# Kernel optimization log

Measured on AMD Instinct MI355X. Metric: run time of the kernel, lower is better.

Reference implementation:

```python
import jax, jax.numpy as jnp
import numpy as np

B, CIN, T = 16, 1024, 2000
BN, OUT, K = 512, 512, 3
DIL = (1, 2, 3)
NBR = len(DIL)
RED = 1
BN_EPS = 1e-5
STD_EPS = 0.01


def setup_inputs() -> dict:
    key = jax.random.key(0)
    ks = jax.random.split(key, 16)
    inp = {
        "x": jax.random.normal(ks[0], (B, CIN, T), dtype=jnp.float32),
        # BatchNorm1d(in_channels) params + running stats (inference mode)
        "bn1_gamma": jax.random.uniform(ks[1], (CIN,), minval=0.5, maxval=1.5),
        "bn1_beta": jax.random.normal(ks[2], (CIN,)) * 0.1,
        "bn1_mean": jax.random.normal(ks[3], (CIN,)) * 0.1,
        "bn1_var": jax.random.uniform(ks[4], (CIN,), minval=0.5, maxval=1.5),
        # linear1: in_channels -> bn_channels, no bias
        "W1": jax.random.normal(ks[5], (BN, CIN)) * (1.0 / np.sqrt(CIN)),
        # BatchNorm1d(bn_channels)
        "bn2_gamma": jax.random.uniform(ks[6], (BN,), minval=0.5, maxval=1.5),
        "bn2_beta": jax.random.normal(ks[7], (BN,)) * 0.1,
        "bn2_mean": jax.random.normal(ks[8], (BN,)) * 0.1,
        "bn2_var": jax.random.uniform(ks[9], (BN,), minval=0.5, maxval=1.5),
        # per-dilation TimeDelay weights [n_branch, OUT, BN, K] (bias=False)
        "conv_w": jax.random.normal(ks[10], (NBR, OUT, BN, K)) * (1.0 / np.sqrt(OUT)),
        # StatsSelect: linear1 (4C -> C//red), linear2 list (C//red -> C)
        "sel_W1": jax.random.normal(ks[11], (OUT // RED, 4 * OUT)) * (1.0 / np.sqrt(4 * OUT)),
        "sel_b1": jax.random.normal(ks[12], (OUT // RED,)) * 0.01,
        "sel_W2": jax.random.normal(ks[13], (NBR, OUT, OUT // RED)) * (1.0 / np.sqrt(OUT // RED)),
        "sel_b2": jax.random.normal(ks[14], (NBR, OUT)) * 0.01,
    }
    return inp


def _bn_relu(x, gamma, beta, mean, var):
    # inference BatchNorm1d over channel dim, then ReLU; x: [B, C, T]
    inv = gamma / jnp.sqrt(var + BN_EPS)
    y = x * inv[None, :, None] + (beta - mean * inv)[None, :, None]
    return jax.nn.relu(y)


def _forward(x, bn1_gamma, bn1_beta, bn1_mean, bn1_var, W1,
             bn2_gamma, bn2_beta, bn2_mean, bn2_var,
             conv_w, sel_W1, sel_b1, sel_W2, sel_b2):
    # bn_function: nonlinear1 -> linear1 (pointwise over channels)
    h = _bn_relu(x, bn1_gamma, bn1_beta, bn1_mean, bn1_var)  # [B, CIN, T]
    h = jnp.einsum('bct,oc->bot', h, W1)                      # [B, BN, T]
    h = _bn_relu(h, bn2_gamma, bn2_beta, bn2_mean, bn2_var)
    # multi-dilation TDNN branches (dilated conv1d with 'same' padding)
    pad = (K - 1) // 2
    outs = []
    for i, d in enumerate(DIL):
        y = jax.lax.conv_general_dilated(
            h, conv_w[i], window_strides=(1,), padding=[(pad * d, pad * d)],
            rhs_dilation=(d,), dimension_numbers=('NCH', 'OIH', 'NCH'))
        outs.append(y)
    f = jnp.stack(outs, axis=1)  # [B, n, OUT, T]
    xs = jnp.sum(f, axis=1)      # [B, OUT, T]
    # high-order statistics pooling over time
    mean = jnp.mean(xs, axis=-1)                     # [B, OUT]
    std = jnp.std(xs, axis=-1, ddof=1)               # unbiased
    norm = (xs - mean[..., None]) / jnp.clip(std, STD_EPS)[..., None]
    skew = jnp.mean(norm ** 3, axis=-1)
    kurt = jnp.mean(norm ** 4, axis=-1)
    stats = jnp.concatenate([mean, std, skew, kurt], axis=-1)  # [B, 4*OUT]
    z = stats @ sel_W1.T + sel_b1                               # [B, OUT//RED]
    s = jnp.einsum('br,ncr->bnc', z, sel_W2) + sel_b2[None]     # [B, n, OUT]
    s = jax.nn.softmax(s, axis=1)[..., None]                    # [B, n, OUT, 1]
    return jnp.sum(f * s, axis=1)                               # [B, OUT, T]


def reference(x, bn1_gamma, bn1_beta, bn1_mean, bn1_var, W1,
              bn2_gamma, bn2_beta, bn2_mean, bn2_var,
              conv_w, sel_W1, sel_b1, sel_W2, sel_b2):
    return _forward(x, bn1_gamma, bn1_beta, bn1_mean, bn1_var, W1,
                    bn2_gamma, bn2_beta, bn2_mean, bn2_var,
                    conv_w, sel_W1, sel_b1, sel_W2, sel_b2)
```

## Files before the change

kernel.cpp:

```cpp
#include <hip/hip_runtime.h>
#include <hip/hip_bf16.h>

#define B_    16
#define CIN_  1024
#define T_    2000
#define BN_   512
#define OUT_  512
#define NBR_  3
#define TP_X  2048
#define TP_H  2056
#define HOFF  4

typedef float  f32x4  __attribute__((ext_vector_type(4)));
typedef __bf16 bf16x8 __attribute__((ext_vector_type(8)));
typedef unsigned short u16;
typedef u16 u16x4 __attribute__((ext_vector_type(4)));
typedef u16 u16x8 __attribute__((ext_vector_type(8)));

static __device__ __forceinline__ float b2f(u16 u) {
    union { float f; unsigned int i; } v; v.i = ((unsigned int)u) << 16; return v.f;
}
static __device__ __forceinline__ u16 f2b(float f) {
    __hip_bfloat16 h = __float2bfloat16(f);
    u16 r; __builtin_memcpy(&r, &h, 2); return r;
}
static __device__ __forceinline__ void gld16(const u16* g, u16* l) {
    __builtin_amdgcn_global_load_lds(
        (const __attribute__((address_space(1))) unsigned int*)g,
        (__attribute__((address_space(3))) unsigned int*)l, 16, 0, 0);
}

__global__ __launch_bounds__(256) void k_prep_x(
    const float* __restrict__ x, const float* __restrict__ g,
    const float* __restrict__ be, const float* __restrict__ mu,
    const float* __restrict__ va, u16* __restrict__ xbT)
{
    __shared__ float tile[32][33];
    int b = blockIdx.z, c0 = blockIdx.y * 32, t0 = blockIdx.x * 32;
    int tid = threadIdx.x;
    int cl = tid >> 3, tt = (tid & 7) * 4;
    int c = c0 + cl;
    float inv = g[c] / sqrtf(va[c] + 1e-5f);
    float bia = be[c] - mu[c] * inv;
    int t = t0 + tt;
    float y0 = 0.f, y1 = 0.f, y2 = 0.f, y3 = 0.f;
    if (t < T_) {
        float4 v = *reinterpret_cast<const float4*>(x + (size_t)(b * CIN_ + c) * T_ + t);
        y0 = fmaxf(v.x * inv + bia, 0.f);
        y1 = fmaxf(v.y * inv + bia, 0.f);
        y2 = fmaxf(v.z * inv + bia, 0.f);
        y3 = fmaxf(v.w * inv + bia, 0.f);
    }
    tile[tt + 0][cl] = y0; tile[tt + 1][cl] = y1;
    tile[tt + 2][cl] = y2; tile[tt + 3][cl] = y3;
    __syncthreads();
    int tl = tid >> 3, c8 = (tid & 7) * 4;
    u16x4 o;
    o.x = f2b(tile[tl][c8 + 0]);
    o.y = f2b(tile[tl][c8 + 1]);
    o.z = f2b(tile[tl][c8 + 2]);
    o.w = f2b(tile[tl][c8 + 3]);
    *reinterpret_cast<u16x4*>(xbT + (size_t)(b * TP_X + t0 + tl) * CIN_ + c0 + c8) = o;
}

__global__ __launch_bounds__(256) void k_prep_w1(
    const float* __restrict__ W1, const float* __restrict__ g,
    const float* __restrict__ be, const float* __restrict__ mu,
    const float* __restrict__ va, u16* __restrict__ W1b, float* __restrict__ bias2)
{
    int i = blockIdx.x * 256 + threadIdx.x;
    int o = i >> 8;
    int c = (i & 255) * 4;
    float inv = g[o] / sqrtf(va[o] + 1e-5f);
    if (c == 0) bias2[o] = be[o] - mu[o] * inv;
    float4 w = *reinterpret_cast<const float4*>(W1 + (size_t)o * CIN_ + c);
    u16x4 r;
    r.x = f2b(w.x * inv); r.y = f2b(w.y * inv);
    r.z = f2b(w.z * inv); r.w = f2b(w.w * inv);
    *reinterpret_cast<u16x4*>(W1b + (size_t)o * CIN_ + c) = r;
}

__global__ __launch_bounds__(256) void k_prep_wc(
    const float* __restrict__ cw, u16* __restrict__ wb)
{
    int i = blockIdx.x * 256 + threadIdx.x;
    if (i >= NBR_ * OUT_ * BN_) return;
    const float* p = cw + (size_t)i * 3;
    int c = i & 511;
    int o = (i >> 9) & 511;
    int n = i >> 18;
#pragma unroll
    for (int k = 0; k < 3; k++)
        wb[((size_t)(n * 3 + k) * OUT_ + o) * BN_ + c] = f2b(p[k]);
}

__global__ __launch_bounds__(256) void k_zero_hpad(u16* __restrict__ hT)
{
    int i = blockIdx.x * 256 + threadIdx.x;
    if (i >= B_ * 56 * BN_) return;
    int c = i & 511;
    int p = (i >> 9) % 56;
    int b = i / (56 * 512);
    int idx = (p < HOFF) ? p : (p + 2000);
    hT[(size_t)(b * TP_H + idx) * BN_ + c] = 0;
}

__global__ __launch_bounds__(256) void k_gemm1(
    const u16* __restrict__ W1b, const u16* __restrict__ xbT,
    const float* __restrict__ bias2, u16* __restrict__ hT)
{
    __shared__ u16 As[128 * 32];
    __shared__ u16 Bs[128 * 32];
    int tid = threadIdx.x;
    int t0 = blockIdx.x * 128;
    int o0 = blockIdx.y * 128;
    int b  = blockIdx.z;
    int lane = tid & 63, wv = tid >> 6;
    int m_off = (wv & 1) * 64, n_off = (wv >> 1) * 64;
    int lr = lane & 15, g = lane >> 4;

    int s0 = wv * 128 + lane, s1 = s0 + 64;
    size_t ga0 = (size_t)(s0 >> 2) * CIN_ + (((s0 & 3) ^ ((s0 >> 3) & 3)) * 8);
    size_t ga1 = (size_t)(s1 >> 2) * CIN_ + (((s1 & 3) ^ ((s1 >> 3) & 3)) * 8);
    u16* lA0 = As + (size_t)(wv * 128) * 8; u16* lA1 = lA0 + 512;
    u16* lB0 = Bs + (size_t)(wv * 128) * 8; u16* lB1 = lB0 + 512;

    int sw = (g ^ ((lr >> 1) & 3)) * 8;
    int fA[4], fB[4];
#pragma unroll
    for (int m = 0; m < 4; m++) fA[m] = (m_off + m * 16 + lr) * 32 + sw;
#pragma unroll
    for (int n = 0; n < 4; n++) fB[n] = (n_off + n * 16 + lr) * 32 + sw;

    f32x4 zz = {0.f, 0.f, 0.f, 0.f};
    f32x4 acc[4][4];
#pragma unroll
    for (int m = 0; m < 4; m++)
#pragma unroll
        for (int n = 0; n < 4; n++) acc[m][n] = zz;

    const u16* Ag = W1b + (size_t)o0 * CIN_;
    const u16* Bg = xbT + (size_t)(b * TP_X + t0) * CIN_;

    for (int kc = 0; kc < CIN_; kc += 32) {
        gld16(Ag + ga0 + kc, lA0);
        gld16(Ag + ga1 + kc, lA1);
        gld16(Bg + ga0 + kc, lB0);
        gld16(Bg + ga1 + kc, lB1);
        __syncthreads();
        bf16x8 af[4], bfr[4];
#pragma unroll
        for (int m = 0; m < 4; m++) af[m] = *reinterpret_cast<const bf16x8*>(As + fA[m]);
#pragma unroll
        for (int n = 0; n < 4; n++) bfr[n] = *reinterpret_cast<const bf16x8*>(Bs + fB[n]);
#pragma unroll
        for (int m = 0; m < 4; m++)
#pragma unroll
            for (int n = 0; n < 4; n++)
                acc[m][n] = __builtin_amdgcn_mfma_f32_16x16x32_bf16(af[m], bfr[n], acc[m][n], 0, 0, 0);
        __syncthreads();
    }

    int qr = (lane >> 4) * 4;
#pragma unroll
    for (int m = 0; m < 4; m++) {
        int o = o0 + m_off + m * 16 + qr;
        f32x4 bb = *reinterpret_cast<const f32x4*>(bias2 + o);
#pragma unroll
        for (int n = 0; n < 4; n++) {
            int t = t0 + n_off + n * 16 + lr;
            if (t < T_) {
                f32x4 v = acc[m][n];
                u16x4 r;
                r.x = f2b(fmaxf(v.x + bb.x, 0.f));
                r.y = f2b(fmaxf(v.y + bb.y, 0.f));
                r.z = f2b(fmaxf(v.z + bb.z, 0.f));
                r.w = f2b(fmaxf(v.w + bb.w, 0.f));
                *reinterpret_cast<u16x4*>(hT + (size_t)(b * TP_H + t + HOFF) * BN_ + o) = r;
            }
        }
    }
}

__global__ __launch_bounds__(256) void k_conv(
    const u16* __restrict__ hT, const u16* __restrict__ wb, u16* __restrict__ f)
{
    __shared__ u16 As[128 * 32];
    __shared__ u16 Bs[128 * 32];
    int tid = threadIdx.x;
    int t0 = blockIdx.x * 128;
    int o0 = blockIdx.y * 128;
    int nb = blockIdx.z;
    int n = nb >> 4, b = nb & 15;
    int d = n + 1;
    int lane = tid & 63, wv = tid >> 6;
    int m_off = (wv & 1) * 64, n_off = (wv >> 1) * 64;
    int lr = lane & 15, g = lane >> 4;

    int s0 = wv * 128 + lane, s1 = s0 + 64;
    size_t ga0 = (size_t)(s0 >> 2) * BN_ + (((s0 & 3) ^ ((s0 >> 3) & 3)) * 8);
    size_t ga1 = (size_t)(s1 >> 2) * BN_ + (((s1 & 3) ^ ((s1 >> 3) & 3)) * 8);
    u16* lA0 = As + (size_t)(wv * 128) * 8; u16* lA1 = lA0 + 512;
    u16* lB0 = Bs + (size_t)(wv * 128) * 8; u16* lB1 = lB0 + 512;

    int sw = (g ^ ((lr >> 1) & 3)) * 8;
    int fA[4], fB[4];
#pragma unroll
    for (int m = 0; m < 4; m++) fA[m] = (m_off + m * 16 + lr) * 32 + sw;
#pragma unroll
    for (int nn = 0; nn < 4; nn++) fB[nn] = (n_off + nn * 16 + lr) * 32 + sw;

    f32x4 zz = {0.f, 0.f, 0.f, 0.f};
    f32x4 acc[4][4];
#pragma unroll
    for (int m = 0; m < 4; m++)
#pragma unroll
        for (int nn = 0; nn < 4; nn++) acc[m][nn] = zz;

    for (int tap = 0; tap < 3; tap++) {
        const u16* Ag = hT + (size_t)(b * TP_H + t0 + d * (tap - 1) + HOFF) * BN_;
        const u16* Bg = wb + (size_t)((n * 3 + tap) * OUT_ + o0) * BN_;
        for (int kc = 0; kc < BN_; kc += 32) {
            gld16(Ag + ga0 + kc, lA0);
            gld16(Ag + ga1 + kc, lA1);
            gld16(Bg + ga0 + kc, lB0);
            gld16(Bg + ga1 + kc, lB1);
            __syncthreads();
            bf16x8 af[4], bfr[4];
#pragma unroll
            for (int m = 0; m < 4; m++) af[m] = *reinterpret_cast<const bf16x8*>(As + fA[m]);
#pragma unroll
            for (int nn = 0; nn < 4; nn++) bfr[nn] = *reinterpret_cast<const bf16x8*>(Bs + fB[nn]);
#pragma unroll
            for (int m = 0; m < 4; m++)
#pragma unroll
                for (int nn = 0; nn < 4; nn++)
                    acc[m][nn] = __builtin_amdgcn_mfma_f32_16x16x32_bf16(af[m], bfr[nn], acc[m][nn], 0, 0, 0);
            __syncthreads();
        }
    }

    int qr = (lane >> 4) * 4;
#pragma unroll
    for (int m = 0; m < 4; m++) {
        int t = t0 + m_off + m * 16 + qr;
#pragma unroll
        for (int nn = 0; nn < 4; nn++) {
            int o = o0 + n_off + nn * 16 + lr;
            f32x4 v = acc[m][nn];
            u16* dst = f + ((size_t)(n * B_ + b) * OUT_ + o) * T_ + t;
            if (t + 3 < T_) {
                u16x4 r;
                r.x = f2b(v.x); r.y = f2b(v.y); r.z = f2b(v.z); r.w = f2b(v.w);
                *reinterpret_cast<u16x4*>(dst) = r;
            } else {
                if (t + 0 < T_) dst[0] = f2b(v.x);
                if (t + 1 < T_) dst[1] = f2b(v.y);
                if (t + 2 < T_) dst[2] = f2b(v.z);
                if (t + 3 < T_) dst[3] = f2b(v.w);
            }
        }
    }
}

__global__ __launch_bounds__(256) void k_stats(
    const u16* __restrict__ f, float* __restrict__ stats)
{
    int bo = blockIdx.x;
    int tid = threadIdx.x;
    const size_t stride = (size_t)B_ * OUT_ * T_;
    const u16* p0 = f + (size_t)bo * T_;
    const u16* p1 = p0 + stride;
    const u16* p2 = p1 + stride;
    double s1 = 0, s2 = 0, s3 = 0, s4 = 0;
    for (int t = tid; t < T_; t += 256) {
        float v = b2f(p0[t]) + b2f(p1[t]) + b2f(p2[t]);
        double dd = (double)v, d2 = dd * dd;
        s1 += dd; s2 += d2; s3 += d2 * dd; s4 += d2 * d2;
    }
    for (int off = 32; off > 0; off >>= 1) {
        s1 += __shfl_down(s1, off);
        s2 += __shfl_down(s2, off);
        s3 += __shfl_down(s3, off);
        s4 += __shfl_down(s4, off);
    }
    __shared__ double red[4][4];
    int lane = tid & 63, wv = tid >> 6;
    if (lane == 0) { red[wv][0] = s1; red[wv][1] = s2; red[wv][2] = s3; red[wv][3] = s4; }
    __syncthreads();
    if (tid == 0) {
        double a1 = 0, a2 = 0, a3 = 0, a4 = 0;
        for (int w = 0; w < 4; w++) { a1 += red[w][0]; a2 += red[w][1]; a3 += red[w][2]; a4 += red[w][3]; }
        const double Tn = (double)T_;
        double m1 = a1 / Tn, m2 = a2 / Tn, m3 = a3 / Tn, m4 = a4 / Tn;
        double c2 = m2 - m1 * m1; if (c2 < 0) c2 = 0;
        double stdv = sqrt(c2 * (Tn / (Tn - 1.0)));
        double sc = stdv > 0.01 ? stdv : 0.01;
        double c3 = m3 - 3.0 * m1 * m2 + 2.0 * m1 * m1 * m1;
        double c4 = m4 - 4.0 * m1 * m3 + 6.0 * m1 * m1 * m2 - 3.0 * m1 * m1 * m1 * m1;
        int b = bo >> 9, o = bo & 511;
        float* sp = stats + (size_t)b * 2048;
        sp[o]        = (float)m1;
        sp[512 + o]  = (float)stdv;
        sp[1024 + o] = (float)(c3 / (sc * sc * sc));
        sp[1536 + o] = (float)(c4 / (sc * sc * sc * sc));
    }
}

__global__ __launch_bounds__(256) void k_sel1(
    const float* __restrict__ stats, const float* __restrict__ W1s,
    const float* __restrict__ b1s, float* __restrict__ z)
{
    int gid = blockIdx.x * 4 + (threadIdx.x >> 6);
    int lane = threadIdx.x & 63;
    int b = gid >> 9, r = gid & 511;
    const float4* wp = reinterpret_cast<const float4*>(W1s + (size_t)r * 2048 + lane * 32);
    const float4* sp = reinterpret_cast<const float4*>(stats + (size_t)b * 2048 + lane * 32);
    float acc = 0.f;
#pragma unroll
    for (int j = 0; j < 8; j++) {
        float4 w = wp[j], s = sp[j];
        acc += w.x * s.x + w.y * s.y + w.z * s.z + w.w * s.w;
    }
#pragma unroll
    for (int off = 32; off > 0; off >>= 1) acc += __shfl_down(acc, off);
    if (lane == 0) z[gid] = acc + b1s[r];
}

__global__ __launch_bounds__(256) void k_sel2(
    const float* __restrict__ z, const float* __restrict__ W2s,
    const float* __restrict__ b2s, float* __restrict__ s)
{
    int gid = blockIdx.x * 4 + (threadIdx.x >> 6);
    int lane = threadIdx.x & 63;
    int b = gid >> 9, c = gid & 511;
    const float4* zp = reinterpret_cast<const float4*>(z + (size_t)b * 512 + lane * 8);
    float4 z0 = zp[0], z1 = zp[1];
    float a[3];
#pragma unroll
    for (int n = 0; n < 3; n++) {
        const float4* wp = reinterpret_cast<const float4*>(W2s + (size_t)(n * 512 + c) * 512 + lane * 8);
        float4 w0 = wp[0], w1 = wp[1];
        float acc = z0.x * w0.x + z0.y * w0.y + z0.z * w0.z + z0.w * w0.w
                  + z1.x * w1.x + z1.y * w1.y + z1.z * w1.z + z1.w * w1.w;
#pragma unroll
        for (int off = 32; off > 0; off >>= 1) acc += __shfl_down(acc, off);
        a[n] = acc + b2s[n * 512 + c];
    }
    if (lane == 0) {
        float mx = fmaxf(a[0], fmaxf(a[1], a[2]));
        float e0 = expf(a[0] - mx), e1 = expf(a[1] - mx), e2 = expf(a[2] - mx);
        float inv = 1.f / (e0 + e1 + e2);
        s[(b * 3 + 0) * 512 + c] = e0 * inv;
        s[(b * 3 + 1) * 512 + c] = e1 * inv;
        s[(b * 3 + 2) * 512 + c] = e2 * inv;
    }
}

__global__ __launch_bounds__(256) void k_final(
    const u16* __restrict__ f, const float* __restrict__ s, float* __restrict__ out)
{
    int id = blockIdx.x * 256 + threadIdx.x;
    int row = id / 250;
    int t = (id % 250) * 8;
    int b = row >> 9, o = row & 511;
    const size_t stride = (size_t)B_ * OUT_ * T_;
    size_t base = (size_t)row * T_ + t;
    float s0 = s[(b * 3 + 0) * 512 + o];
    float s1 = s[(b * 3 + 1) * 512 + o];
    float s2 = s[(b * 3 + 2) * 512 + o];
    u16x8 a0 = *reinterpret_cast<const u16x8*>(f + base);
    u16x8 a1 = *reinterpret_cast<const u16x8*>(f + stride + base);
    u16x8 a2 = *reinterpret_cast<const u16x8*>(f + 2 * stride + base);
    float4 r0, r1;
    r0.x = s0 * b2f(a0[0]) + s1 * b2f(a1[0]) + s2 * b2f(a2[0]);
    r0.y = s0 * b2f(a0[1]) + s1 * b2f(a1[1]) + s2 * b2f(a2[1]);
    r0.z = s0 * b2f(a0[2]) + s1 * b2f(a1[2]) + s2 * b2f(a2[2]);
    r0.w = s0 * b2f(a0[3]) + s1 * b2f(a1[3]) + s2 * b2f(a2[3]);
    r1.x = s0 * b2f(a0[4]) + s1 * b2f(a1[4]) + s2 * b2f(a2[4]);
    r1.y = s0 * b2f(a0[5]) + s1 * b2f(a1[5]) + s2 * b2f(a2[5]);
    r1.z = s0 * b2f(a0[6]) + s1 * b2f(a1[6]) + s2 * b2f(a2[6]);
    r1.w = s0 * b2f(a0[7]) + s1 * b2f(a1[7]) + s2 * b2f(a2[7]);
    *reinterpret_cast<float4*>(out + base)     = r0;
    *reinterpret_cast<float4*>(out + base + 4) = r1;
}

extern "C" void kernel_launch(void* const* d_in, const int* in_sizes, int n_in,
                              void* d_out, int out_size, void* d_ws, size_t ws_size,
                              hipStream_t stream)
{
    const float* x     = (const float*)d_in[0];
    const float* bn1g  = (const float*)d_in[1];
    const float* bn1b  = (const float*)d_in[2];
    const float* bn1m  = (const float*)d_in[3];
    const float* bn1v  = (const float*)d_in[4];
    const float* W1    = (const float*)d_in[5];
    const float* bn2g  = (const float*)d_in[6];
    const float* bn2b  = (const float*)d_in[7];
    const float* bn2m  = (const float*)d_in[8];
    const float* bn2v  = (const float*)d_in[9];
    const float* convw = (const float*)d_in[10];
    const float* selW1 = (const float*)d_in[11];
    const float* selb1 = (const float*)d_in[12];
    const float* selW2 = (const float*)d_in[13];
    const float* selb2 = (const float*)d_in[14];
    float* out = (float*)d_out;

    char* ws = (char*)d_ws;
    u16*   xbT   = (u16*)(ws);
    u16*   hT    = (u16*)(ws + 67108864);
    u16*   W1b   = (u16*)(ws + 100794368);
    float* bias2 = (float*)(ws + 101842944);
    u16*   wb    = (u16*)(ws + 101844992);
    u16*   fbuf  = (u16*)(ws + 106563584);
    float* stats = (float*)(ws + 204867584);
    float* zbuf  = (float*)(ws + 204998656);
    float* sbuf  = (float*)(ws + 205031424);

    k_prep_x  <<<dim3(64, 32, 16), 256, 0, stream>>>(x, bn1g, bn1b, bn1m, bn1v, xbT);
    k_prep_w1 <<<512,  256, 0, stream>>>(W1, bn2g, bn2b, bn2m, bn2v, W1b, bias2);
    k_prep_wc <<<3072, 256, 0, stream>>>(convw, wb);
    k_zero_hpad<<<1792, 256, 0, stream>>>(hT);
    k_gemm1   <<<dim3(16, 4, 16), 256, 0, stream>>>(W1b, xbT, bias2, hT);
    k_conv    <<<dim3(16, 4, 48), 256, 0, stream>>>(hT, wb, fbuf);
    k_stats   <<<8192, 256, 0, stream>>>(fbuf, stats);
    k_sel1    <<<2048, 256, 0, stream>>>(stats, selW1, selb1, zbuf);
    k_sel2    <<<2048, 256, 0, stream>>>(zbuf, selW2, selb2, sbuf);
    k_final   <<<8000, 256, 0, stream>>>(fbuf, sbuf, out);
}
```

Measured before the change: 565.1 us.

## Share one halo A tile across conv taps, vectorize stats loads, alias fbuf over xbT

The dilated conv kernel now loads a single A tile of time rows plus a halo (128+2d rows) per K-chunk and reads all three taps from it at shifted row offsets. It also loads all three tap weight tiles at once, which cuts A-side global traffic and the number of barriers per K-chunk by a factor of three. The stats kernel reads 8 bf16 values per thread with vector loads instead of strided scalar loads. The workspace is repacked so fbuf aliases the dead xbT region, and the hT padding grows to cover the extra halo rows. Costs are larger LDS use (about 9 KB for A and 24 KB for B), which may lower occupancy, and the stats kernel assumes 16-byte alignment of each row.

```diff
diff --git a/kernel.cpp b/kernel.cpp
--- a/kernel.cpp
+++ b/kernel.cpp
@@ -8,7 +8,7 @@
 #define OUT_  512
 #define NBR_  3
 #define TP_X  2048
-#define TP_H  2056
+#define TP_H  2064
 #define HOFF  4
 
 typedef float  f32x4  __attribute__((ext_vector_type(4)));
@@ -97,10 +97,10 @@
 __global__ __launch_bounds__(256) void k_zero_hpad(u16* __restrict__ hT)
 {
     int i = blockIdx.x * 256 + threadIdx.x;
-    if (i >= B_ * 56 * BN_) return;
+    if (i >= B_ * 64 * BN_) return;
     int c = i & 511;
-    int p = (i >> 9) % 56;
-    int b = i / (56 * 512);
+    int p = (i >> 9) % 64;
+    int b = i / (64 * 512);
     int idx = (p < HOFF) ? p : (p + 2000);
     hT[(size_t)(b * TP_H + idx) * BN_ + c] = 0;
 }
@@ -185,8 +185,8 @@
 __global__ __launch_bounds__(256) void k_conv(
     const u16* __restrict__ hT, const u16* __restrict__ wb, u16* __restrict__ f)
 {
-    __shared__ u16 As[128 * 32];
-    __shared__ u16 Bs[128 * 32];
+    __shared__ u16 As[576 * 8];
+    __shared__ u16 Bs[3 * 512 * 8];
     int tid = threadIdx.x;
     int t0 = blockIdx.x * 128;
     int o0 = blockIdx.y * 128;
@@ -197,16 +197,19 @@
     int m_off = (wv & 1) * 64, n_off = (wv >> 1) * 64;
     int lr = lane & 15, g = lane >> 4;
 
-    int s0 = wv * 128 + lane, s1 = s0 + 64;
-    size_t ga0 = (size_t)(s0 >> 2) * BN_ + (((s0 & 3) ^ ((s0 >> 3) & 3)) * 8);
-    size_t ga1 = (size_t)(s1 >> 2) * BN_ + (((s1 & 3) ^ ((s1 >> 3) & 3)) * 8);
-    u16* lA0 = As + (size_t)(wv * 128) * 8; u16* lA1 = lA0 + 512;
-    u16* lB0 = Bs + (size_t)(wv * 128) * 8; u16* lB1 = lB0 + 512;
+    int q1 = tid + 256;
+    size_t off0 = (size_t)(tid >> 2) * BN_ + (((tid & 3) ^ ((tid >> 3) & 3)) * 8);
+    size_t off1 = (size_t)(q1 >> 2) * BN_ + (((q1 & 3) ^ ((q1 >> 3) & 3)) * 8);
+    int q2 = 512 + (lane & 31);
+    size_t off2 = (size_t)(q2 >> 2) * BN_ + (((q2 & 3) ^ ((q2 >> 3) & 3)) * 8);
+    u16* lA0 = As + (size_t)(wv * 64) * 8;
+    u16* lA1 = As + (size_t)(256 + wv * 64) * 8;
+    u16* lA2 = As + (size_t)512 * 8;
+    u16* lB0 = Bs + (size_t)(wv * 64) * 8;
+    u16* lB1 = Bs + (size_t)(256 + wv * 64) * 8;
 
     int sw = (g ^ ((lr >> 1) & 3)) * 8;
-    int fA[4], fB[4];
-#pragma unroll
-    for (int m = 0; m < 4; m++) fA[m] = (m_off + m * 16 + lr) * 32 + sw;
+    int fB[4];
 #pragma unroll
     for (int nn = 0; nn < 4; nn++) fB[nn] = (n_off + nn * 16 + lr) * 32 + sw;
 
@@ -217,27 +220,42 @@
 #pragma unroll
         for (int nn = 0; nn < 4; nn++) acc[m][nn] = zz;
 
-    for (int tap = 0; tap < 3; tap++) {
-        const u16* Ag = hT + (size_t)(b * TP_H + t0 + d * (tap - 1) + HOFF) * BN_;
-        const u16* Bg = wb + (size_t)((n * 3 + tap) * OUT_ + o0) * BN_;
-        for (int kc = 0; kc < BN_; kc += 32) {
-            gld16(Ag + ga0 + kc, lA0);
-            gld16(Ag + ga1 + kc, lA1);
-            gld16(Bg + ga0 + kc, lB0);
-            gld16(Bg + ga1 + kc, lB1);
-            __syncthreads();
+    const u16* Agh = hT + (size_t)(b * TP_H + t0 - d + HOFF) * BN_;
+    const u16* Bg[3];
+#pragma unroll
+    for (int tap = 0; tap < 3; tap++)
+        Bg[tap] = wb + (size_t)((n * 3 + tap) * OUT_ + o0) * BN_;
+
+    for (int kc = 0; kc < BN_; kc += 32) {
+        gld16(Agh + off0 + kc, lA0);
+        gld16(Agh + off1 + kc, lA1);
+        if (wv == 0) gld16(Agh + off2 + kc, lA2);
+#pragma unroll
+        for (int tap = 0; tap < 3; tap++) {
+            gld16(Bg[tap] + off0 + kc, lB0 + tap * 4096);
+            gld16(Bg[tap] + off1 + kc, lB1 + tap * 4096);
+        }
+        __syncthreads();
+#pragma unroll
+        for (int tap = 0; tap < 3; tap++) {
+            int rsh = d * tap;
             bf16x8 af[4], bfr[4];
 #pragma unroll
-            for (int m = 0; m < 4; m++) af[m] = *reinterpret_cast<const bf16x8*>(As + fA[m]);
-#pragma unroll
-            for (int nn = 0; nn < 4; nn++) bfr[nn] = *reinterpret_cast<const bf16x8*>(Bs + fB[nn]);
+            for (int m = 0; m < 4; m++) {
+                int row = m_off + m * 16 + lr + rsh;
+                af[m] = *reinterpret_cast<const bf16x8*>(
+                    As + row * 32 + ((g ^ ((row >> 1) & 3)) * 8));
+            }
+#pragma unroll
+            for (int nn = 0; nn < 4; nn++)
+                bfr[nn] = *reinterpret_cast<const bf16x8*>(Bs + tap * 4096 + fB[nn]);
 #pragma unroll
             for (int m = 0; m < 4; m++)
 #pragma unroll
                 for (int nn = 0; nn < 4; nn++)
                     acc[m][nn] = __builtin_amdgcn_mfma_f32_16x16x32_bf16(af[m], bfr[nn], acc[m][nn], 0, 0, 0);
-            __syncthreads();
         }
+        __syncthreads();
     }
 
     int qr = (lane >> 4) * 4;
@@ -269,14 +287,18 @@
     int bo = blockIdx.x;
     int tid = threadIdx.x;
     const size_t stride = (size_t)B_ * OUT_ * T_;
-    const u16* p0 = f + (size_t)bo * T_;
-    const u16* p1 = p0 + stride;
-    const u16* p2 = p1 + stride;
     double s1 = 0, s2 = 0, s3 = 0, s4 = 0;
-    for (int t = tid; t < T_; t += 256) {
-        float v = b2f(p0[t]) + b2f(p1[t]) + b2f(p2[t]);
-        double dd = (double)v, d2 = dd * dd;
-        s1 += dd; s2 += d2; s3 += d2 * dd; s4 += d2 * d2;
+    if (tid < 250) {
+        const u16* p0 = f + (size_t)bo * T_ + tid * 8;
+        u16x8 a0 = *reinterpret_cast<const u16x8*>(p0);
+        u16x8 a1 = *reinterpret_cast<const u16x8*>(p0 + stride);
+        u16x8 a2 = *reinterpret_cast<const u16x8*>(p0 + 2 * stride);
+#pragma unroll
+        for (int j = 0; j < 8; j++) {
+            float v = b2f(a0[j]) + b2f(a1[j]) + b2f(a2[j]);
+            double dd = (double)v, d2 = dd * dd;
+            s1 += dd; s2 += d2; s3 += d2 * dd; s4 += d2 * d2;
+        }
     }
     for (int off = 32; off > 0; off >>= 1) {
         s1 += __shfl_down(s1, off);
@@ -407,20 +429,20 @@
     float* out = (float*)d_out;
 
     char* ws = (char*)d_ws;
+    u16*   fbuf  = (u16*)(ws);
     u16*   xbT   = (u16*)(ws);
-    u16*   hT    = (u16*)(ws + 67108864);
-    u16*   W1b   = (u16*)(ws + 100794368);
-    float* bias2 = (float*)(ws + 101842944);
-    u16*   wb    = (u16*)(ws + 101844992);
-    u16*   fbuf  = (u16*)(ws + 106563584);
-    float* stats = (float*)(ws + 204867584);
-    float* zbuf  = (float*)(ws + 204998656);
-    float* sbuf  = (float*)(ws + 205031424);
+    u16*   hT    = (u16*)(ws + 98304000);
+    u16*   W1b   = (u16*)(ws + 132120576);
+    float* bias2 = (float*)(ws + 133169152);
+    u16*   wb    = (u16*)(ws + 133171200);
+    float* stats = (float*)(ws + 137889792);
+    float* zbuf  = (float*)(ws + 138020864);
+    float* sbuf  = (float*)(ws + 138053632);
 
     k_prep_x  <<<dim3(64, 32, 16), 256, 0, stream>>>(x, bn1g, bn1b, bn1m, bn1v, xbT);
     k_prep_w1 <<<512,  256, 0, stream>>>(W1, bn2g, bn2b, bn2m, bn2v, W1b, bias2);
     k_prep_wc <<<3072, 256, 0, stream>>>(convw, wb);
-    k_zero_hpad<<<1792, 256, 0, stream>>>(hT);
+    k_zero_hpad<<<2048, 256, 0, stream>>>(hT);
     k_gemm1   <<<dim3(16, 4, 16), 256, 0, stream>>>(W1b, xbT, bias2, hT);
     k_conv    <<<dim3(16, 4, 48), 256, 0, stream>>>(hT, wb, fbuf);
     k_stats   <<<8192, 256, 0, stream>>>(fbuf, stats);
```

After: 504.7 us. 10.7% less time.
